# Kernel optimization log

Measured on AMD Instinct MI355X. Metric: run time of the kernel, lower is better.

The kernel has to match this reference:

```python
import jax, jax.numpy as jnp
import numpy as np

B, T, N, C_IN = 2, 12, 50000, 1
H = 16          # hidden = out channels of STConv
KT = 3          # temporal kernel size
E = 800000      # edges (avg degree 16)
NUM_CLASSES = 2


def _temporal_conv(x, wP, bP, wQ, bQ, wR, bR):
    # Gated temporal conv (GLU): relu(P * sigmoid(Q) + R), 'valid' conv over time.
    # x: (B, Tt, N, C); w*: (KT, C, H)
    Tt = x.shape[1]
    def conv(w, b):
        out = b
        for k in range(KT):  # KT=3, tiny unrolled loop
            out = out + jnp.einsum('btnc,co->btno', x[:, k:Tt - KT + 1 + k], w[k])
        return out
    return jax.nn.relu(conv(wP, bP) * jax.nn.sigmoid(conv(wQ, bQ)) + conv(wR, bR))


def _cheb_conv(x, edge_index, edge_weight, w, b):
    # ChebConv K=2, sym normalization, lambda_max=2:
    #   out  = Tx_0 @ W0 + Tx_1 @ W1 + b
    src, dst = edge_index[0], edge_index[1]
    n = x.shape[2]
    deg = jax.ops.segment_sum(edge_weight, src, num_segments=n)
    dis = jnp.where(deg > 0, jax.lax.rsqrt(jnp.maximum(deg, 1e-12)), 0.0)
    norm = -dis[src] * edge_weight * dis[dst]                    # (E,)
    Bc, Tc, _, Hc = x.shape
    xf = jnp.transpose(x, (2, 0, 1, 3)).reshape(n, -1)           # (N, B*T*H)
    agg = jax.ops.segment_sum(norm[:, None] * xf[src], dst, num_segments=n)
    tx1 = jnp.transpose(agg.reshape(n, Bc, Tc, Hc), (1, 2, 0, 3))  # (B, T, N, H)
    return jnp.einsum('btnc,co->btno', x, w[0]) + jnp.einsum('btnc,co->btno', tx1, w[1]) + b


def _forward(x, edge_index, edge_weight,
             tc1_P_w, tc1_P_b, tc1_Q_w, tc1_Q_b, tc1_R_w, tc1_R_b,
             cheb_w, cheb_b,
             tc2_P_w, tc2_P_b, tc2_Q_w, tc2_Q_b, tc2_R_w, tc2_R_b,
             lin_w, lin_b):
    h = _temporal_conv(x, tc1_P_w, tc1_P_b, tc1_Q_w, tc1_Q_b, tc1_R_w, tc1_R_b)  # (B, T-2, N, H)
    h = jax.nn.relu(_cheb_conv(h, edge_index, edge_weight, cheb_w, cheb_b))
    h = _temporal_conv(h, tc2_P_w, tc2_P_b, tc2_Q_w, tc2_Q_b, tc2_R_w, tc2_R_b)  # (B, T-4, N, H)
    h = h.mean(axis=1)                                                            # (B, N, H)
    return h @ lin_w + lin_b                                                      # (B, N, classes)


def setup_inputs() -> dict:
    key = jax.random.key(0)
    ks = jax.random.split(key, 12)
    x = jax.random.normal(ks[0], (B, T, N, C_IN), jnp.float32)
    edge_index = jax.random.randint(ks[1], (2, E), 0, N, dtype=jnp.int32).astype(jnp.int64)
    edge_weight = jax.random.uniform(ks[2], (E,), jnp.float32)

    def conv_w(k, cin, cout):
        s = 1.0 / np.sqrt(cin * KT)
        return jax.random.uniform(k, (KT, cin, cout), jnp.float32, -s, s)

    inp = {'x': x, 'edge_index': edge_index, 'edge_weight': edge_weight}
    for i, name in enumerate(['tc1_P', 'tc1_Q', 'tc1_R']):
        inp[name + '_w'] = conv_w(ks[3 + i], C_IN, H)
        inp[name + '_b'] = jnp.zeros((H,), jnp.float32)
    for i, name in enumerate(['tc2_P', 'tc2_Q', 'tc2_R']):
        inp[name + '_w'] = conv_w(ks[6 + i], H, H)
        inp[name + '_b'] = jnp.zeros((H,), jnp.float32)
    sc = 1.0 / np.sqrt(H)
    inp['cheb_w'] = jax.random.uniform(ks[9], (2, H, H), jnp.float32, -sc, sc)
    inp['cheb_b'] = jnp.zeros((H,), jnp.float32)
    inp['lin_w'] = jax.random.uniform(ks[10], (H, NUM_CLASSES), jnp.float32, -sc, sc)
    inp['lin_b'] = jnp.zeros((NUM_CLASSES,), jnp.float32)
    return inp


def reference(x, edge_index, edge_weight,
              tc1_P_w, tc1_P_b, tc1_Q_w, tc1_Q_b, tc1_R_w, tc1_R_b,
              tc2_P_w, tc2_P_b, tc2_Q_w, tc2_Q_b, tc2_R_w, tc2_R_b,
              cheb_w, cheb_b, lin_w, lin_b):
    return _forward(x, edge_index, edge_weight,
                    tc1_P_w, tc1_P_b, tc1_Q_w, tc1_Q_b, tc1_R_w, tc1_R_b,
                    cheb_w, cheb_b,
                    tc2_P_w, tc2_P_b, tc2_Q_w, tc2_Q_b, tc2_R_w, tc2_R_b,
                    lin_w, lin_b)
```

## Files before the change

kernel.cpp:

```cpp
#include <hip/hip_runtime.h>

typedef unsigned short ushort_t;
typedef unsigned int uint_t;
typedef __attribute__((ext_vector_type(8))) short short8;
typedef __attribute__((ext_vector_type(4))) float float4v;

constexpr int Bb = 2, Tt = 12, Nn = 50000, Hh = 16, Ee = 800000;
constexpr int T1 = 10, T2 = 8;
constexpr int F = 320;
constexpr int NP = 50176;
constexpr int CAP = 64;

#define DEV __device__ __forceinline__

DEV float bf2f(ushort_t u) { return __uint_as_float(((uint_t)u) << 16); }
DEV ushort_t f2bf(float f) {
  uint_t u = __float_as_uint(f);
  u += 0x7fffu + ((u >> 16) & 1u);
  return (ushort_t)(u >> 16);
}
DEV float blo(uint_t u) { return __uint_as_float(u << 16); }
DEV float bhi(uint_t u) { return __uint_as_float(u & 0xffff0000u); }
DEV float sigm(float x) { return 1.0f / (1.0f + __expf(-x)); }

DEV float loadF(const void* p, int j, int isb) {
  return isb ? bf2f(((const ushort_t*)p)[j]) : ((const float*)p)[j];
}
DEV int loadI(const void* p, long long j, int is64) {
  return is64 ? (int)(((const long long*)p)[j]) : ((const int*)p)[j];
}

__global__ void k_wprep(const void* ew, const void* ei,
                        const void* t1Pw, const void* t1Pb,
                        const void* t1Qw, const void* t1Qb,
                        const void* t1Rw, const void* t1Rb,
                        const void* t2Pw, const void* t2Pb,
                        const void* t2Qw, const void* t2Qb,
                        const void* t2Rw, const void* t2Rb,
                        const void* chw, const void* chb,
                        const void* lw, const void* lb,
                        int* flags, float* W, ushort_t* Bf, uint_t* zero_base) {
  int gid = blockIdx.x * 256 + threadIdx.x;
  if (gid < 9 * NP) zero_base[gid] = 0u;
  if (blockIdx.x != 0) return;

  __shared__ int sflags[2];
  int tid = threadIdx.x;
  if (tid < 64) {
    int lane = tid;
    const ushort_t* u = (const ushort_t*)ew;
    int cnt = 0;
    for (int j = lane; j < 512; j += 64) cnt += (u[j] < 0x3F80u) ? 1 : 0;
#pragma unroll
    for (int d = 32; d; d >>= 1) cnt += __shfl_xor(cnt, d, 64);
    const int* e32 = (const int*)ei;
    int even_nz = 0, odd_nz = 0;
    for (int j = 2 * lane; j < 256; j += 128) {
      even_nz |= (e32[j] != 0);
      odd_nz |= (e32[j + 1] != 0);
    }
    unsigned long long be = __ballot(even_nz), bo = __ballot(odd_nz);
    if (lane == 0) {
      int f0 = (cnt >= 450) ? 1 : 0;
      int f1 = (bo == 0ull && be != 0ull) ? 1 : 0;
      sflags[0] = f0; sflags[1] = f1;
      flags[0] = f0; flags[1] = f1;
    }
  }
  __syncthreads();
  int isb = sflags[0];
#define CVT(src, off, n) for (int j = tid; j < (n); j += 256) W[(off) + j] = loadF(src, j, isb);
  CVT(t1Pw, 0, 48)   CVT(t1Pb, 48, 16)
  CVT(t1Qw, 64, 48)  CVT(t1Qb, 112, 16)
  CVT(t1Rw, 128, 48) CVT(t1Rb, 176, 16)
  CVT(t2Pw, 192, 768)  CVT(t2Pb, 960, 16)
  CVT(t2Qw, 976, 768)  CVT(t2Qb, 1744, 16)
  CVT(t2Rw, 1760, 768) CVT(t2Rb, 2528, 16)
  CVT(chw, 2544, 512)  CVT(chb, 3056, 16)
  CVT(lw, 3072, 32)    CVT(lb, 3104, 2)
#undef CVT
  for (int i = tid; i < 3072; i += 256) {
    int j = i & 7, lane = (i >> 3) & 63, s = (i >> 9) & 1, tau = i >> 10;
    int kap = s * 32 + ((lane >> 4) << 3) + j;
    int nsub = lane & 15;
    ushort_t v = 0;
    if (kap < 48) {
      int kk = kap >> 4, c = kap & 15;
      const void* src = (tau == 0) ? t2Pw : (tau == 1) ? t2Qw : t2Rw;
      v = f2bf(loadF(src, kk * 256 + c * 16 + nsub, isb));
    }
    Bf[i] = v;
  }
}

__global__ __launch_bounds__(256) void k_pre(const void* __restrict__ x,
                                             const void* __restrict__ ei,
                                             const void* __restrict__ ew,
                                             const float* __restrict__ W,
                                             const int* __restrict__ flags,
                                             ushort_t* __restrict__ xfh,
                                             float* __restrict__ deg8,
                                             int* __restrict__ cnt,
                                             uint_t* __restrict__ ecv) {
  int id = blockIdx.x * 256 + threadIdx.x;
  int isb = flags[0];
  if (id < Ee) {
    int is64 = flags[1];
    int s = loadI(ei, id, is64), d = loadI(ei, (long long)Ee + id, is64);
    float w = loadF(ew, id, isb);
    atomicAdd(&deg8[(blockIdx.x & 7) * NP + s], w);
    int pos = atomicAdd(&cnt[d], 1);
    if (pos < CAP) ecv[d * CAP + pos] = ((uint_t)s << 16) | (uint_t)f2bf(w);
  }
  if (id < Bb * T1 * Nn) {
    int n = id % Nn;
    int bt = id / Nn;
    int t = bt % T1, b = bt / T1;
    float x0 = loadF(x, (b * Tt + t + 0) * Nn + n, isb);
    float x1 = loadF(x, (b * Tt + t + 1) * Nn + n, isb);
    float x2 = loadF(x, (b * Tt + t + 2) * Nn + n, isb);
    ushort_t g[16];
#pragma unroll
    for (int h = 0; h < 16; ++h) {
      float p = W[48 + h] + x0 * W[0 + h] + x1 * W[16 + h] + x2 * W[32 + h];
      float q = W[112 + h] + x0 * W[64 + h] + x1 * W[80 + h] + x2 * W[96 + h];
      float r = W[176 + h] + x0 * W[128 + h] + x1 * W[144 + h] + x2 * W[160 + h];
      g[h] = f2bf(fmaxf(fmaf(p, sigm(q), r), 0.0f));
    }
    uint_t u[8];
#pragma unroll
    for (int j = 0; j < 8; ++j) u[j] = (uint_t)g[2 * j] | ((uint_t)g[2 * j + 1] << 16);
    uint4* dst = (uint4*)(xfh + (size_t)n * F + t * 32 + b * 16);
    dst[0] = make_uint4(u[0], u[1], u[2], u[3]);
    dst[1] = make_uint4(u[4], u[5], u[6], u[7]);
  }
}

__global__ __launch_bounds__(256) void k_dis(float* __restrict__ deg8) {
  int i = blockIdx.x * 256 + threadIdx.x;
  if (i >= Nn) return;
  float v = 0.0f;
#pragma unroll
  for (int j = 0; j < 8; ++j) v += deg8[j * NP + i];
  deg8[i] = (v > 0.0f) ? (1.0f / sqrtf(fmaxf(v, 1e-12f))) : 0.0f;
}

__global__ __launch_bounds__(256) void k_agg(const int* __restrict__ cnt,
                                             const uint_t* __restrict__ ecv,
                                             const float* __restrict__ dis,
                                             const uint2* __restrict__ xf2,
                                             const float* __restrict__ W,
                                             ushort_t* __restrict__ h2) {
  __shared__ float sh[4][640];
  int wid = threadIdx.x >> 6;
  int lane = threadIdx.x & 63;
  int gw = blockIdx.x * 4 + wid;
  int deg = min(cnt[gw], CAP);
  int l16 = 64 + (lane & 15);
  float a0 = 0.f, a1 = 0.f, a2 = 0.f, a3 = 0.f;
  float c0 = 0.f, c1 = 0.f, c2 = 0.f, c3 = 0.f;

#define ACC(v, p, q)                                                          \
  a0 = fmaf(v, blo(p.x), a0); a1 = fmaf(v, bhi(p.x), a1);                     \
  a2 = fmaf(v, blo(p.y), a2); a3 = fmaf(v, bhi(p.y), a3);                     \
  c0 = fmaf(v, blo(q.x), c0); c1 = fmaf(v, bhi(q.x), c1);                     \
  c2 = fmaf(v, blo(q.y), c2); c3 = fmaf(v, bhi(q.y), c3);

  int colv = 0; float valv = 0.0f;
  if (lane < deg) {
    uint_t t = ecv[gw * CAP + lane];
    int src = t >> 16;
    colv = src * 80;
    valv = bf2f((ushort_t)(t & 0xffffu)) * dis[src];
  }
  int e = 0;
  for (; e + 4 <= deg; e += 4) {
    int r0 = __shfl(colv, e + 0), r1 = __shfl(colv, e + 1);
    int r2 = __shfl(colv, e + 2), r3 = __shfl(colv, e + 3);
    float v0 = __shfl(valv, e + 0), v1 = __shfl(valv, e + 1);
    float v2 = __shfl(valv, e + 2), v3 = __shfl(valv, e + 3);
    uint2 p0 = xf2[r0 + lane], q0 = xf2[r0 + l16];
    uint2 p1 = xf2[r1 + lane], q1 = xf2[r1 + l16];
    uint2 p2 = xf2[r2 + lane], q2 = xf2[r2 + l16];
    uint2 p3 = xf2[r3 + lane], q3 = xf2[r3 + l16];
    ACC(v0, p0, q0) ACC(v1, p1, q1) ACC(v2, p2, q2) ACC(v3, p3, q3)
  }
  for (; e < deg; ++e) {
    int r = __shfl(colv, e);
    float v = __shfl(valv, e);
    uint2 p = xf2[r + lane], q = xf2[r + l16];
    ACC(v, p, q)
  }
#undef ACC

  float nd = -dis[gw];
  float* sa = sh[wid];
  float* sx = sh[wid] + 320;
  const uint2* xrow = xf2 + (size_t)gw * 80;
  uint2 xp = xrow[lane], xq = xrow[l16];
  ((float4*)sa)[lane] = make_float4(a0 * nd, a1 * nd, a2 * nd, a3 * nd);
  ((float4*)sx)[lane] = make_float4(blo(xp.x), bhi(xp.x), blo(xp.y), bhi(xp.y));
  if (lane < 16) {
    ((float4*)sa)[64 + lane] = make_float4(c0 * nd, c1 * nd, c2 * nd, c3 * nd);
    ((float4*)sx)[64 + lane] = make_float4(blo(xq.x), bhi(xq.x), blo(xq.y), bhi(xq.y));
  }
  __builtin_amdgcn_wave_barrier();
  int h = lane & 15;
  float w0[16], w1[16];
#pragma unroll
  for (int c = 0; c < 16; ++c) {
    w0[c] = W[2544 + c * 16 + h];
    w1[c] = W[2800 + c * 16 + h];
  }
  float bias = W[3056 + h];
  ushort_t* orow = h2 + (size_t)gw * F;
#pragma unroll
  for (int j = 0; j < 5; ++j) {
    int base2 = (lane & 48) + 64 * j;
    float o2 = bias;
#pragma unroll
    for (int c = 0; c < 16; ++c)
      o2 = fmaf(sx[base2 + c], w0[c], fmaf(sa[base2 + c], w1[c], o2));
    orow[lane + 64 * j] = f2bf(fmaxf(o2, 0.0f));
  }
}

__global__ __launch_bounds__(256) void k_tc2h(const ushort_t* __restrict__ h2,
                                              const ushort_t* __restrict__ Bf,
                                              const float* __restrict__ W,
                                              float* __restrict__ out) {
  int tid = threadIdx.x;
  int wid = tid >> 6, lane = tid & 63;
  int quad = lane >> 4, hcol = lane & 15;
  short8 bfr[3][2];
#pragma unroll
  for (int tau = 0; tau < 3; ++tau)
#pragma unroll
    for (int s = 0; s < 2; ++s)
      bfr[tau][s] = *(const short8*)(Bf + (tau * 1024 + s * 512 + lane * 8));
  float pb = W[960 + hcol], qb = W[1744 + hcol], rb = W[2528 + hcol];
  float lw0 = W[3072 + 2 * hcol], lw1 = W[3073 + 2 * hcol];
  float ob0 = W[3104], ob1 = W[3105];
  int bm = hcol >> 3, t2m = hcol & 7;
  int kk0 = quad >> 1, off0 = (quad & 1) * 8;
#pragma unroll
  for (int nn = 0; nn < 4; ++nn) {
    int n = blockIdx.x * 16 + wid * 4 + nn;
    const ushort_t* row = h2 + (size_t)n * F;
    short8 a0 = *(const short8*)(row + (t2m + kk0) * 32 + bm * 16 + off0);
    short8 a1 = (short8)0;
    if (quad < 2) a1 = *(const short8*)(row + (t2m + 2) * 32 + bm * 16 + quad * 8);
    float4v accP = {0.f, 0.f, 0.f, 0.f};
    float4v accQ = {0.f, 0.f, 0.f, 0.f};
    float4v accR = {0.f, 0.f, 0.f, 0.f};
    accP = __builtin_amdgcn_mfma_f32_16x16x32_bf16(a0, bfr[0][0], accP, 0, 0, 0);
    accP = __builtin_amdgcn_mfma_f32_16x16x32_bf16(a1, bfr[0][1], accP, 0, 0, 0);
    accQ = __builtin_amdgcn_mfma_f32_16x16x32_bf16(a0, bfr[1][0], accQ, 0, 0, 0);
    accQ = __builtin_amdgcn_mfma_f32_16x16x32_bf16(a1, bfr[1][1], accQ, 0, 0, 0);
    accR = __builtin_amdgcn_mfma_f32_16x16x32_bf16(a0, bfr[2][0], accR, 0, 0, 0);
    accR = __builtin_amdgcn_mfma_f32_16x16x32_bf16(a1, bfr[2][1], accR, 0, 0, 0);
    float s0 = 0.0f;
#pragma unroll
    for (int r = 0; r < 4; ++r) {
      float P = accP[r] + pb, Q = accQ[r] + qb, R = accR[r] + rb;
      s0 += fmaxf(fmaf(P, sigm(Q), R), 0.0f);
    }
    s0 += __shfl_xor(s0, 16);
    float mmean = s0 * 0.125f;
    float u0 = mmean * lw0, u1 = mmean * lw1;
#pragma unroll
    for (int d = 1; d < 16; d <<= 1) {
      u0 += __shfl_xor(u0, d);
      u1 += __shfl_xor(u1, d);
    }
    if ((lane & 31) == 0) {
      int b = lane >> 5;
      ((float2*)out)[(size_t)b * Nn + n] = make_float2(u0 + ob0, u1 + ob1);
    }
  }
}

extern "C" void kernel_launch(void* const* d_in, const int* in_sizes, int n_in,
                              void* d_out, int out_size, void* d_ws, size_t ws_size,
                              hipStream_t stream) {
  (void)in_sizes; (void)n_in; (void)out_size; (void)ws_size;
  const void* x = d_in[0];
  const void* ei = d_in[1];
  const void* ew = d_in[2];

  char* wsb = (char*)d_ws;
  size_t off = 0;
  auto alloc = [&](size_t bytes) -> void* {
    void* p = wsb + off;
    off = (off + bytes + 255) & ~(size_t)255;
    return p;
  };
  int* flags = (int*)alloc(256);
  float* W = (float*)alloc(4096 * 4);
  ushort_t* Bf = (ushort_t*)alloc(3072 * 2);
  float* deg8 = (float*)alloc((size_t)8 * NP * 4);
  int* cnt = (int*)alloc((size_t)NP * 4);
  uint_t* ecv = (uint_t*)alloc((size_t)Nn * CAP * 4);
  ushort_t* xfh = (ushort_t*)alloc((size_t)Nn * F * 2);
  ushort_t* h2 = (ushort_t*)alloc((size_t)Nn * F * 2);

  int zblk = (9 * NP + 255) / 256;
  k_wprep<<<zblk, 256, 0, stream>>>(
      ew, ei,
      d_in[3], d_in[4], d_in[5], d_in[6], d_in[7], d_in[8],
      d_in[9], d_in[10], d_in[11], d_in[12], d_in[13], d_in[14],
      d_in[15], d_in[16], d_in[17], d_in[18], flags, W, Bf, (uint_t*)deg8);

  k_pre<<<(Bb * T1 * Nn + 255) / 256, 256, 0, stream>>>(x, ei, ew, W, flags, xfh, deg8, cnt, ecv);
  k_dis<<<(Nn + 255) / 256, 256, 0, stream>>>(deg8);
  k_agg<<<Nn / 4, 256, 0, stream>>>(cnt, ecv, deg8, (const uint2*)xfh, W, h2);
  k_tc2h<<<Nn / 16, 256, 0, stream>>>(h2, Bf, W, (float*)d_out);
}
```

Baseline: 288.8 us.

## Partition edge atomics per XCD with workgroup-scope fixed-point accumulation

Degree sums and destination bucket counts are now kept in separate per-XCD copies, indexed by the hardware XCC id. The atomics use workgroup memory scope so they can resolve within each die's L2 rather than at device scope. Degrees are accumulated as 24-bit fixed-point unsigned integers instead of float atomics. The aggregation kernel merges the eight per-XCD edge lists, each capped at 16 entries, with a per-lane prefix over the counts. The cost is extra count reads and more scattered edge-list loads in aggregation. Edges are silently dropped if more than 16 land in one XCD bucket for a node, and the result depends on workgroup-scope atomics staying coherent across workgroups on the same XCD.

Result: faster. 283.0 us (-2.0%).

```diff
diff --git a/kernel.cpp b/kernel.cpp
--- a/kernel.cpp
+++ b/kernel.cpp
@@ -9,7 +9,8 @@
 constexpr int T1 = 10, T2 = 8;
 constexpr int F = 320;
 constexpr int NP = 50176;
-constexpr int CAP = 64;
+constexpr int NXCD = 8;
+constexpr int CAP8 = 16;
 
 #define DEV __device__ __forceinline__
 
@@ -22,6 +23,12 @@
 DEV float blo(uint_t u) { return __uint_as_float(u << 16); }
 DEV float bhi(uint_t u) { return __uint_as_float(u & 0xffff0000u); }
 DEV float sigm(float x) { return 1.0f / (1.0f + __expf(-x)); }
+
+DEV int xcc_id() {
+  int x;
+  asm volatile("s_getreg_b32 %0, hwreg(HW_REG_XCC_ID)" : "=s"(x));
+  return x & (NXCD - 1);
+}
 
 DEV float loadF(const void* p, int j, int isb) {
   return isb ? bf2f(((const ushort_t*)p)[j]) : ((const float*)p)[j];
@@ -41,7 +48,7 @@
                         const void* lw, const void* lb,
                         int* flags, float* W, ushort_t* Bf, uint_t* zero_base) {
   int gid = blockIdx.x * 256 + threadIdx.x;
-  if (gid < 9 * NP) zero_base[gid] = 0u;
+  if (gid < 16 * NP) zero_base[gid] = 0u;
   if (blockIdx.x != 0) return;
 
   __shared__ int sflags[2];
@@ -99,18 +106,23 @@
                                              const float* __restrict__ W,
                                              const int* __restrict__ flags,
                                              ushort_t* __restrict__ xfh,
-                                             float* __restrict__ deg8,
-                                             int* __restrict__ cnt,
-                                             uint_t* __restrict__ ecv) {
+                                             uint_t* __restrict__ deg8,
+                                             int* __restrict__ cnt8,
+                                             uint_t* __restrict__ ecv8) {
   int id = blockIdx.x * 256 + threadIdx.x;
   int isb = flags[0];
   if (id < Ee) {
     int is64 = flags[1];
     int s = loadI(ei, id, is64), d = loadI(ei, (long long)Ee + id, is64);
     float w = loadF(ew, id, isb);
-    atomicAdd(&deg8[(blockIdx.x & 7) * NP + s], w);
-    int pos = atomicAdd(&cnt[d], 1);
-    if (pos < CAP) ecv[d * CAP + pos] = ((uint_t)s << 16) | (uint_t)f2bf(w);
+    int xcd = xcc_id();
+    uint_t wq = __float2uint_rn(w * 16777216.0f);
+    __hip_atomic_fetch_add(&deg8[xcd * NP + s], wq,
+                           __ATOMIC_RELAXED, __HIP_MEMORY_SCOPE_WORKGROUP);
+    int pos = __hip_atomic_fetch_add(&cnt8[xcd * NP + d], 1,
+                                     __ATOMIC_RELAXED, __HIP_MEMORY_SCOPE_WORKGROUP);
+    if (pos < CAP8)
+      ecv8[((size_t)xcd * Nn + d) * CAP8 + pos] = ((uint_t)s << 16) | (uint_t)f2bf(w);
   }
   if (id < Bb * T1 * Nn) {
     int n = id % Nn;
@@ -136,17 +148,18 @@
   }
 }
 
-__global__ __launch_bounds__(256) void k_dis(float* __restrict__ deg8) {
+__global__ __launch_bounds__(256) void k_dis(uint_t* __restrict__ deg8) {
   int i = blockIdx.x * 256 + threadIdx.x;
   if (i >= Nn) return;
-  float v = 0.0f;
+  uint_t v = 0;
 #pragma unroll
   for (int j = 0; j < 8; ++j) v += deg8[j * NP + i];
-  deg8[i] = (v > 0.0f) ? (1.0f / sqrtf(fmaxf(v, 1e-12f))) : 0.0f;
-}
-
-__global__ __launch_bounds__(256) void k_agg(const int* __restrict__ cnt,
-                                             const uint_t* __restrict__ ecv,
+  float f = (float)v * (1.0f / 16777216.0f);
+  ((float*)deg8)[i] = (v > 0u) ? (1.0f / sqrtf(fmaxf(f, 1e-12f))) : 0.0f;
+}
+
+__global__ __launch_bounds__(256) void k_agg(const int* __restrict__ cnt8,
+                                             const uint_t* __restrict__ ecv8,
                                              const float* __restrict__ dis,
                                              const uint2* __restrict__ xf2,
                                              const float* __restrict__ W,
@@ -155,7 +168,14 @@
   int wid = threadIdx.x >> 6;
   int lane = threadIdx.x & 63;
   int gw = blockIdx.x * 4 + wid;
-  int deg = min(cnt[gw], CAP);
+  int myx = 0, slot = lane, tot = 0;
+#pragma unroll
+  for (int xx = 0; xx < NXCD; ++xx) {
+    int c = min(cnt8[xx * NP + gw], CAP8);
+    if (lane >= tot) { myx = xx; slot = lane - tot; }
+    tot += c;
+  }
+  int deg = min(tot, 64);
   int l16 = 64 + (lane & 15);
   float a0 = 0.f, a1 = 0.f, a2 = 0.f, a3 = 0.f;
   float c0 = 0.f, c1 = 0.f, c2 = 0.f, c3 = 0.f;
@@ -168,7 +188,7 @@
 
   int colv = 0; float valv = 0.0f;
   if (lane < deg) {
-    uint_t t = ecv[gw * CAP + lane];
+    uint_t t = ecv8[((size_t)myx * Nn + gw) * CAP8 + slot];
     int src = t >> 16;
     colv = src * 80;
     valv = bf2f((ushort_t)(t & 0xffffu)) * dis[src];
@@ -298,21 +318,21 @@
   int* flags = (int*)alloc(256);
   float* W = (float*)alloc(4096 * 4);
   ushort_t* Bf = (ushort_t*)alloc(3072 * 2);
-  float* deg8 = (float*)alloc((size_t)8 * NP * 4);
-  int* cnt = (int*)alloc((size_t)NP * 4);
-  uint_t* ecv = (uint_t*)alloc((size_t)Nn * CAP * 4);
+  uint_t* deg8 = (uint_t*)alloc((size_t)NXCD * NP * 4);
+  int* cnt8 = (int*)alloc((size_t)NXCD * NP * 4);
+  uint_t* ecv8 = (uint_t*)alloc((size_t)NXCD * Nn * CAP8 * 4);
   ushort_t* xfh = (ushort_t*)alloc((size_t)Nn * F * 2);
   ushort_t* h2 = (ushort_t*)alloc((size_t)Nn * F * 2);
 
-  int zblk = (9 * NP + 255) / 256;
+  int zblk = (16 * NP + 255) / 256;
   k_wprep<<<zblk, 256, 0, stream>>>(
       ew, ei,
       d_in[3], d_in[4], d_in[5], d_in[6], d_in[7], d_in[8],
       d_in[9], d_in[10], d_in[11], d_in[12], d_in[13], d_in[14],
-      d_in[15], d_in[16], d_in[17], d_in[18], flags, W, Bf, (uint_t*)deg8);
-
-  k_pre<<<(Bb * T1 * Nn + 255) / 256, 256, 0, stream>>>(x, ei, ew, W, flags, xfh, deg8, cnt, ecv);
+      d_in[15], d_in[16], d_in[17], d_in[18], flags, W, Bf, deg8);
+
+  k_pre<<<(Bb * T1 * Nn + 255) / 256, 256, 0, stream>>>(x, ei, ew, W, flags, xfh, deg8, cnt8, ecv8);
   k_dis<<<(Nn + 255) / 256, 256, 0, stream>>>(deg8);
-  k_agg<<<Nn / 4, 256, 0, stream>>>(cnt, ecv, deg8, (const uint2*)xfh, W, h2);
+  k_agg<<<Nn / 4, 256, 0, stream>>>(cnt8, ecv8, (const float*)deg8, (const uint2*)xfh, W, h2);
   k_tc2h<<<Nn / 16, 256, 0, stream>>>(h2, Bf, W, (float*)d_out);
 }
```
